# Optimization experiments

Hardware: AMD Instinct MI355X
Metric: run time of the kernel (lower is better)

The kernel has to match this reference:

```python
import jax, jax.numpy as jnp
import numpy as np
import math

N, NF, D, HEADS, LEVELS, POINTS = 1, 2, 256, 8, 4, 4
SPATIAL = np.array([[100, 100], [50, 50], [25, 25], [13, 13]], dtype=np.int32)
LEN_IN = int((SPATIAL[:, 0] * SPATIAL[:, 1]).sum())  # 13294
LEN_Q = LEN_IN


def _grid_init_bias():
    # faithful to MSDeformAttn._reset_parameters
    thetas = np.arange(HEADS, dtype=np.float32) * (2.0 * math.pi / HEADS)
    grid = np.stack([np.cos(thetas), np.sin(thetas)], -1)
    grid = grid / np.abs(grid).max(-1, keepdims=True)
    grid = np.tile(grid.reshape(HEADS, 1, 1, 2), (1, LEVELS, POINTS, 1))
    for i in range(POINTS):
        grid[:, :, i, :] *= i + 1
    return grid.reshape(-1).astype(np.float32)  # [HEADS*LEVELS*POINTS*2]


def setup_inputs() -> dict:
    key = jax.random.key(0)
    ks = jax.random.split(key, 8)
    lsi = np.concatenate([[0], np.cumsum(SPATIAL[:, 0] * SPATIAL[:, 1])[:-1]]).astype(np.int32)
    s = 1.0 / math.sqrt(D)
    return {
        "query": jax.random.normal(ks[0], (N, NF, LEN_Q, D), jnp.float32),
        "reference_points": jax.random.uniform(ks[1], (N, LEN_Q, LEVELS, 2), jnp.float32),
        "input_flatten": jax.random.normal(ks[2], (N, NF, LEN_IN, D), jnp.float32),
        "input_spatial_shapes": jnp.asarray(SPATIAL),
        "input_level_start_index": jnp.asarray(lsi),
        "Wv": jax.random.normal(ks[3], (D, D), jnp.float32) * s,
        "bv": jnp.zeros((D,), jnp.float32),
        "Woff": jax.random.normal(ks[4], (D, HEADS * LEVELS * POINTS * 2), jnp.float32) * 0.01,
        "boff": jnp.asarray(_grid_init_bias()),
        "Wattn": jax.random.normal(ks[5], (D, HEADS * LEVELS * POINTS), jnp.float32) * 0.02,
        "battn": jnp.zeros((HEADS * LEVELS * POINTS,), jnp.float32),
        "Wout": jax.random.normal(ks[6], (D, D), jnp.float32) * s,
        "bout": jnp.zeros((D,), jnp.float32),
    }


def ms_deform_attn_core(value, spatial_shapes, level_start_index, loc, attn):
    """value: [B, Lin, H, Dh]; loc: [B, Lq, H, L, P, 2] in [0,1]; attn: [B, Lq, H, L, P].
    Bilinear sampling matches F.grid_sample(align_corners=False, padding_mode='zeros')
    applied to grid = 2*loc - 1, i.e. pixel coord = loc*size - 0.5."""
    B, Lin, Hn, Dh = value.shape
    Lq, L, P = loc.shape[1], loc.shape[3], loc.shape[4]
    val_t = value.transpose(0, 2, 1, 3)  # [B, H, Lin, Dh]
    out = jnp.zeros((B, Lq, Hn, Dh), value.dtype)
    for l in range(L):
        Hl = spatial_shapes[l, 0]
        Wl = spatial_shapes[l, 1]
        start = level_start_index[l]
        x = loc[:, :, :, l, :, 0] * Wl - 0.5  # [B, Lq, H, P]
        y = loc[:, :, :, l, :, 1] * Hl - 0.5
        x0 = jnp.floor(x)
        y0 = jnp.floor(y)
        lx, ly = x - x0, y - y0
        x0i = x0.astype(jnp.int32)
        y0i = y0.astype(jnp.int32)
        sampled = jnp.zeros((B, Lq, Hn, P, Dh), value.dtype)
        corners = [(0, 0, (1 - lx) * (1 - ly)), (0, 1, lx * (1 - ly)),
                   (1, 0, (1 - lx) * ly), (1, 1, lx * ly)]
        for dy, dx, w in corners:
            xi = x0i + dx
            yi = y0i + dy
            valid = (xi >= 0) & (xi < Wl) & (yi >= 0) & (yi < Hl)
            idx = start + jnp.clip(yi, 0, Hl - 1) * Wl + jnp.clip(xi, 0, Wl - 1)
            idx_t = idx.transpose(0, 2, 1, 3).reshape(B, Hn, Lq * P)  # [B, H, Lq*P]
            v = jnp.take_along_axis(val_t, idx_t[:, :, :, None], axis=2)  # [B, H, Lq*P, Dh]
            v = v.reshape(B, Hn, Lq, P, Dh).transpose(0, 2, 1, 3, 4)  # [B, Lq, H, P, Dh]
            sampled = sampled + jnp.where(valid, w, 0.0)[..., None] * v
        out = out + jnp.einsum('blhp,blhpd->blhd', attn[:, :, :, l, :], sampled)
    return out.reshape(B, Lq, Hn * Dh)


def reference(query, reference_points, input_flatten, input_spatial_shapes,
              input_level_start_index, Wv, bv, Woff, boff, Wattn, battn, Wout, bout):
    n, nf, Lq, d = query.shape
    Lin = input_flatten.shape[2]
    Dh = d // HEADS
    value = (input_flatten @ Wv + bv).reshape(n * nf, Lin, HEADS, Dh)
    off = (query @ Woff + boff).reshape(n, nf, Lq, HEADS, LEVELS, POINTS, 2)
    aw = (query @ Wattn + battn).reshape(n, nf, Lq, HEADS, LEVELS * POINTS)
    aw = jax.nn.softmax(aw, axis=-1).reshape(n, nf, Lq, HEADS, LEVELS, POINTS)
    # offset normalizer: [W, H] per level
    norm = jnp.stack([input_spatial_shapes[:, 1], input_spatial_shapes[:, 0]], -1).astype(query.dtype)
    # reference_points: [n, Lq, L, 2] -> broadcast with offsets [n, nf, Lq, H, L, P, 2]
    loc = reference_points[:, None, :, None, :, None, :] + off / norm[None, None, None, None, :, None, :]
    loc = loc.reshape(n * nf, Lq, HEADS, LEVELS, POINTS, 2)
    aw = aw.reshape(n * nf, Lq, HEADS, LEVELS, POINTS)
    out = ms_deform_attn_core(value, input_spatial_shapes, input_level_start_index, loc, aw)
    out = out.reshape(n, nf, Lq, d)
    return out @ Wout + bout
```

## Files before the change

### kernel.cpp

```cpp
#include <hip/hip_runtime.h>
#include <math.h>

#define LEN_Q 13294
#define LEN_IN 13294
#define NFRAMES 2
#define MTOT (LEN_Q * NFRAMES)
#define HEADS 8
#define LEVELS 4
#define POINTS 4

typedef __attribute__((ext_vector_type(8))) short short8;
typedef __attribute__((ext_vector_type(4))) float f32x4;
typedef __attribute__((ext_vector_type(2))) float f32x2;
typedef __attribute__((ext_vector_type(2))) unsigned int uint2v;
typedef __attribute__((ext_vector_type(4))) unsigned int uint4v;

__device__ __forceinline__ unsigned short f2bf(float x) {
    unsigned u = __builtin_bit_cast(unsigned, x);
    unsigned r = (u + 0x7fffu + ((u >> 16) & 1u)) >> 16;
    return (unsigned short)r;
}
__device__ __forceinline__ float bf2f(unsigned short b) {
    return __builtin_bit_cast(float, (unsigned)b << 16);
}
__device__ __forceinline__ float bfl(unsigned u) {
    return __builtin_bit_cast(float, u << 16);
}
__device__ __forceinline__ float bfh(unsigned u) {
    return __builtin_bit_cast(float, u & 0xffff0000u);
}
__device__ __forceinline__ short8 pack8(f32x4 x0, f32x4 x1) {
    short8 p;
    p[0]=(short)f2bf(x0.x); p[1]=(short)f2bf(x0.y); p[2]=(short)f2bf(x0.z); p[3]=(short)f2bf(x0.w);
    p[4]=(short)f2bf(x1.x); p[5]=(short)f2bf(x1.y); p[6]=(short)f2bf(x1.z); p[7]=(short)f2bf(x1.w);
    return p;
}

__device__ __forceinline__ void gld_lds16(const unsigned short* g, unsigned short* l) {
    __builtin_amdgcn_global_load_lds(
        (const __attribute__((address_space(1))) void*)g,
        (__attribute__((address_space(3))) void*)l, 16, 0, 0);
}

__device__ __forceinline__ void stage_tile(const unsigned short* __restrict__ g,
                                           unsigned short* lds, int t) {
    const unsigned short* ga = g + (t >> 2) * 256 + (t & 3) * 8;
    gld_lds16(ga, lds + t * 8);
    gld_lds16(ga + 64 * 256, lds + 2048 + t * 8);
}

#define CONV_BLOCKS 2048
__global__ __launch_bounds__(256) void prep_all(
    const float* __restrict__ Wv,  const float* __restrict__ Woff,
    const float* __restrict__ Wat, const float* __restrict__ Wout,
    unsigned short* __restrict__ wvT,
    unsigned short* __restrict__ woaT,
    unsigned short* __restrict__ woutT,
    const float* __restrict__ a, const float* __restrict__ b,
    unsigned short* __restrict__ oa, unsigned short* __restrict__ ob)
{
    const int blk = blockIdx.x;
    const int k = threadIdx.x;
    if (blk < 896) {
        const float* src; unsigned short* dst; int N; int n;
        if (blk < 256)      { src = Wv;   dst = wvT;          N = 256; n = blk; }
        else if (blk < 512) { src = Woff; dst = woaT;         N = 256; n = blk - 256; }
        else if (blk < 640) { src = Wat;  dst = woaT + 65536; N = 128; n = blk - 512; }
        else                { src = Wout; dst = woutT;        N = 256; n = blk - 640; }
        dst[(size_t)n * 256 + k] = f2bf(src[(size_t)k * N + n]);
        return;
    }
    size_t gid = (size_t)(blk - 896) * 256 + k;
    size_t stride = (size_t)CONV_BLOCKS * 256;
    const size_t n8 = (size_t)MTOT * 256 / 8;
    for (size_t i = gid; i < n8; i += stride) {
        size_t off = i * 8;
        f32x4 x0 = *(const f32x4*)(a + off);
        f32x4 x1 = *(const f32x4*)(a + off + 4);
        *(short8*)(oa + off) = pack8(x0, x1);
        f32x4 y0 = *(const f32x4*)(b + off);
        f32x4 y1 = *(const f32x4*)(b + off + 4);
        *(short8*)(ob + off) = pack8(y0, y1);
    }
}

#define CSTR 136
__global__ __launch_bounds__(256) void gemm_fused5(
    const unsigned short* __restrict__ A16v,
    const unsigned short* __restrict__ A16q,
    const unsigned short* __restrict__ BTv,
    const unsigned short* __restrict__ BToa,
    const float* __restrict__ bv,
    const float* __restrict__ boff,
    const float* __restrict__ battn,
    unsigned short* __restrict__ vdup,
    unsigned short* __restrict__ off16,
    unsigned short* __restrict__ at16,
    int M)
{
    __shared__ __align__(16) unsigned char shraw[24576];
    unsigned short* As = (unsigned short*)shraw;
    unsigned short* Bs = (unsigned short*)(shraw + 8192);
    unsigned short* Cs = (unsigned short*)shraw;

    const int t = threadIdx.x;
    const int w = t >> 6;
    const int L = t & 63;

    const int bid = blockIdx.x;
    const int xcd = bid & 7;
    const int kk = bid >> 3;
    const int nt = kk % 5;
    const int m0 = ((kk / 5) * 8 + xcd) * 64;

    const unsigned short* Abase = ((nt < 2) ? A16v : A16q) + (size_t)m0 * 256;
    const unsigned short* Bbase = (nt < 2) ? (BTv + (size_t)nt * 128 * 256)
                                           : (BToa + (size_t)(nt - 2) * 128 * 256);

    const int mq = (w & 1) * 32;
    const int nq = (w >> 1) * 64;
    const int lr = L & 15;
    const int kq = (L >> 4) * 8;

    f32x4 acc[2][4];
    #pragma unroll
    for (int i = 0; i < 2; ++i)
        #pragma unroll
        for (int j = 0; j < 4; ++j) acc[i][j] = (f32x4){0.f, 0.f, 0.f, 0.f};

    gld_lds16(Abase + (t >> 2) * 256 + (t & 3) * 8, As + t * 8);
    stage_tile(Bbase, Bs, t);

    #pragma unroll
    for (int ks = 0; ks < 8; ++ks) {
        const int cur = ks & 1;
        __syncthreads();
        if (ks < 7) {
            gld_lds16(Abase + (ks + 1) * 32 + (t >> 2) * 256 + (t & 3) * 8,
                      As + (cur ^ 1) * 2048 + t * 8);
            stage_tile(Bbase + (ks + 1) * 32, Bs + (cur ^ 1) * 4096, t);
        }
        short8 af[2], bf[4];
        #pragma unroll
        for (int i = 0; i < 2; ++i)
            af[i] = *(const short8*)&As[cur * 2048 + (mq + i * 16 + lr) * 32 + kq];
        #pragma unroll
        for (int j = 0; j < 4; ++j)
            bf[j] = *(const short8*)&Bs[cur * 4096 + (nq + j * 16 + lr) * 32 + kq];
        #pragma unroll
        for (int i = 0; i < 2; ++i)
            #pragma unroll
            for (int j = 0; j < 4; ++j)
                acc[i][j] = __builtin_amdgcn_mfma_f32_16x16x32_bf16(af[i], bf[j], acc[i][j], 0, 0, 0);
    }

    __syncthreads();

    const int rr = (L >> 4) * 4;
    {
        float bj[4];
        #pragma unroll
        for (int j = 0; j < 4; ++j) {
            int colg = nt * 128 + nq + j * 16 + lr;
            bj[j] = (colg < 256) ? bv[colg]
                  : (colg < 512) ? boff[colg - 256] : battn[colg - 512];
        }
        #pragma unroll
        for (int i = 0; i < 2; ++i)
            #pragma unroll
            for (int r = 0; r < 4; ++r) {
                int mloc = mq + i * 16 + rr + r;
                #pragma unroll
                for (int j = 0; j < 4; ++j)
                    Cs[mloc * CSTR + nq + j * 16 + lr] = f2bf(acc[i][j][r] + bj[j]);
            }
    }
    __syncthreads();

    if (nt < 2) {
        #pragma unroll
        for (int it = 0; it < 4; ++it) {
            int idx = it * 256 + t;
            int row = idx >> 4;
            int rem = idx & 15;
            int hh_loc = rem >> 2;
            int cc = rem & 3;
            int m = m0 + row;
            if (m < M) {
                int fr = (m >= LEN_Q) ? 1 : 0;
                int e = m - fr * LEN_Q;
                int hh = nt * 4 + hh_loc;
                uint4v v = *(const uint4v*)&Cs[row * CSTR + hh_loc * 32 + cc * 8];
                size_t eb = ((size_t)(fr * 8 + hh) * (LEN_IN + 1) + e) * 64;
                *(uint4v*)&vdup[eb + cc * 8] = v;
                if (e > 0) *(uint4v*)&vdup[eb - 64 + 32 + cc * 8] = v;
            }
        }
    } else if (nt < 4) {
        #pragma unroll
        for (int it = 0; it < 4; ++it) {
            int idx = it * 256 + t;
            int row = idx >> 4;
            int c16 = idx & 15;
            int m = m0 + row;
            if (m < M) {
                uint4v v = *(const uint4v*)&Cs[row * CSTR + c16 * 8];
                *(uint4v*)&off16[(size_t)m * 256 + (nt - 2) * 128 + c16 * 8] = v;
            }
        }
    } else {
        #pragma unroll
        for (int it = 0; it < 4; ++it) {
            int idx = it * 256 + t;
            int row = idx >> 4;
            int c16 = idx & 15;
            int m = m0 + row;
            if (m < M) {
                uint4v v = *(const uint4v*)&Cs[row * CSTR + c16 * 8];
                *(uint4v*)&at16[(size_t)m * 128 + c16 * 8] = v;
            }
        }
    }
}

#define OSTR 132
__global__ __launch_bounds__(256) void gemm_out4(
    const unsigned short* __restrict__ A,
    const unsigned short* __restrict__ BT,
    const float* __restrict__ bias,
    float* __restrict__ C,
    int M)
{
    __shared__ __align__(16) unsigned char raw[64 * OSTR * 4];
    unsigned short* As = (unsigned short*)raw;
    unsigned short* Bs = (unsigned short*)(raw + 8192);
    float* Cs = (float*)raw;

    const int t = threadIdx.x;
    const int w = t >> 6;
    const int L = t & 63;

    const int bid = blockIdx.x;
    const int xcd = bid & 7;
    const int kk = bid >> 3;
    const int nt = kk & 1;
    const int m0 = (((kk >> 1) * 8) + xcd) * 64;
    const int n0 = nt * 128;

    const unsigned short* Abase = A + (size_t)m0 * 256;
    const unsigned short* Bbase = BT + (size_t)n0 * 256;

    const int mq = (w & 1) * 32;
    const int nq = (w >> 1) * 64;
    const int lr = L & 15;
    const int kq = (L >> 4) * 8;

    f32x4 acc[2][4];
    #pragma unroll
    for (int i = 0; i < 2; ++i)
        #pragma unroll
        for (int j = 0; j < 4; ++j) acc[i][j] = (f32x4){0.f, 0.f, 0.f, 0.f};

    gld_lds16(Abase + (t >> 2) * 256 + (t & 3) * 8, As + t * 8);
    stage_tile(Bbase, Bs, t);

    #pragma unroll
    for (int ks = 0; ks < 8; ++ks) {
        const int cur = ks & 1;
        __syncthreads();
        if (ks < 7) {
            gld_lds16(Abase + (ks + 1) * 32 + (t >> 2) * 256 + (t & 3) * 8,
                      As + (cur ^ 1) * 2048 + t * 8);
            stage_tile(Bbase + (ks + 1) * 32, Bs + (cur ^ 1) * 4096, t);
        }
        short8 af[2], bf[4];
        #pragma unroll
        for (int i = 0; i < 2; ++i)
            af[i] = *(const short8*)&As[cur * 2048 + (mq + i * 16 + lr) * 32 + kq];
        #pragma unroll
        for (int j = 0; j < 4; ++j)
            bf[j] = *(const short8*)&Bs[cur * 4096 + (nq + j * 16 + lr) * 32 + kq];
        #pragma unroll
        for (int i = 0; i < 2; ++i)
            #pragma unroll
            for (int j = 0; j < 4; ++j)
                acc[i][j] = __builtin_amdgcn_mfma_f32_16x16x32_bf16(af[i], bf[j], acc[i][j], 0, 0, 0);
    }

    __syncthreads();

    const int rr = (L >> 4) * 4;
    {
        float bj[4];
        #pragma unroll
        for (int j = 0; j < 4; ++j) bj[j] = bias[n0 + nq + j * 16 + lr];
        #pragma unroll
        for (int i = 0; i < 2; ++i)
            #pragma unroll
            for (int r = 0; r < 4; ++r) {
                int mloc = mq + i * 16 + rr + r;
                #pragma unroll
                for (int j = 0; j < 4; ++j)
                    Cs[mloc * OSTR + nq + j * 16 + lr] = acc[i][j][r] + bj[j];
            }
    }
    __syncthreads();

    #pragma unroll
    for (int it = 0; it < 8; ++it) {
        int idx = it * 256 + t;
        int row = idx >> 5;
        int c = idx & 31;
        int m = m0 + row;
        if (m < M) {
            f32x4 v = *(const f32x4*)&Cs[row * OSTR + c * 4];
            *(f32x4*)(C + (size_t)m * 256 + n0 + c * 4) = v;
        }
    }
}

__global__ __launch_bounds__(256) void sample12(
    const unsigned short* __restrict__ vdup,
    const unsigned short* __restrict__ off,
    const unsigned short* __restrict__ attn,
    const float* __restrict__ refpts,
    const int*   __restrict__ spatial,
    const int*   __restrict__ lsi,
    unsigned short* __restrict__ samp)
{
    const int b = blockIdx.x;
    const int h = b & 7;
    const int chunk = b >> 3;
    const int t = threadIdx.x;
    const int rl = t >> 3;
    const int j = t & 7;

    int row = chunk * 32 + rl;
    const bool valid = row < MTOT;
    if (row > MTOT - 1) row = MTOT - 1;
    const int frame = row >= LEN_Q ? 1 : 0;
    const int q = row - frame * LEN_Q;

    __shared__ float w_s[32][68];
    __shared__ int   b_s[32][20];

    uint2v ov = *(const uint2v*)(off + (size_t)row * 256 + h * 32 + j * 4);
    unsigned av = *(const unsigned*)(attn + (size_t)row * 128 + h * 16 + j * 2);
    float t0 = bf2f((unsigned short)(av & 0xffffu));
    float t1 = bf2f((unsigned short)(av >> 16));

    float m = fmaxf(t0, t1);
    #pragma unroll
    for (int d = 1; d < 8; d <<= 1) m = fmaxf(m, __shfl_xor(m, d));
    float e0 = __expf(t0 - m);
    float e1 = __expf(t1 - m);
    float s = e0 + e1;
    #pragma unroll
    for (int d = 1; d < 8; d <<= 1) s += __shfl_xor(s, d);
    float inv = 1.f / s;
    float wt01[2] = { e0 * inv, e1 * inv };

    {
        const int l = j >> 1;
        const int Hl = spatial[l * 2], Wl = spatial[l * 2 + 1];
        const int start = lsi[l];
        const int slab = (frame * 8 + h) * (LEN_IN + 1);
        const float rx = refpts[((size_t)q * LEVELS + l) * 2];
        const float ry = refpts[((size_t)q * LEVELS + l) * 2 + 1];
        #pragma unroll
        for (int i = 0; i < 2; ++i) {
            const int lp = 2 * j + i;
            unsigned sel = (i == 0) ? ov.x : ov.y;
            float ox = bf2f((unsigned short)(sel & 0xffffu));
            float oy = bf2f((unsigned short)(sel >> 16));
            float locx = rx + ox * __builtin_amdgcn_rcpf((float)Wl);
            float locy = ry + oy * __builtin_amdgcn_rcpf((float)Hl);
            float wt = wt01[i];
            float x = locx * (float)Wl - 0.5f;
            float y = locy * (float)Hl - 0.5f;
            float x0f = floorf(x), y0f = floorf(y);
            float lx = x - x0f, ly = y - y0f;
            int x0 = (int)x0f, y0 = (int)y0f;
            int xbase = min(max(x0, 0), Wl - 2);
            int ybase = min(max(y0, 0), Hl - 2);
            float wxe0 = (x0 == xbase) ? (1.f - lx) : ((x0 == -1) ? lx : 0.f);
            float wxe1 = (x0 == xbase) ? lx : ((x0 == Wl - 1) ? (1.f - lx) : 0.f);
            float wye0 = (y0 == ybase) ? (1.f - ly) : ((y0 == -1) ? ly : 0.f);
            float wye1 = (y0 == ybase) ? ly : ((y0 == Hl - 1) ? (1.f - ly) : 0.f);
            b_s[rl][lp] = (slab + start + ybase * Wl + xbase) * 128;
            f32x4 wv;
            wv.x = wt * wxe0 * wye0;
            wv.y = wt * wxe0 * wye1;
            wv.z = wt * wxe1 * wye0;
            wv.w = wt * wxe1 * wye1;
            *(f32x4*)&w_s[rl][lp * 4] = wv;
        }
    }
    __syncthreads();

    const char* vb = (const char*)vdup;
    const unsigned lane16 = (unsigned)(j * 16);
    const int hi2 = ((j >> 2) & 1) * 2;
    int ystr[4];
    #pragma unroll
    for (int l2 = 0; l2 < 4; ++l2) ystr[l2] = spatial[l2 * 2 + 1] * 128;

    f32x2  wbuf[3][2];
    uint4v vbuf[3][4];
    auto fetch = [&](int buf, int g) {
        wbuf[buf][0] = *(const f32x2*)&w_s[rl][(2 * g) * 4 + hi2];
        wbuf[buf][1] = *(const f32x2*)&w_s[rl][(2 * g + 1) * 4 + hi2];
        int b0 = b_s[rl][2 * g];
        int b1 = b_s[rl][2 * g + 1];
        int ys = ystr[g >> 1];
        vbuf[buf][0] = *(const uint4v*)(vb + (unsigned)b0 + lane16);
        vbuf[buf][1] = *(const uint4v*)(vb + (unsigned)(b0 + ys) + lane16);
        vbuf[buf][2] = *(const uint4v*)(vb + (unsigned)b1 + lane16);
        vbuf[buf][3] = *(const uint4v*)(vb + (unsigned)(b1 + ys) + lane16);
    };

    f32x2 a2[4];
    #pragma unroll
    for (int k = 0; k < 4; ++k) a2[k] = (f32x2){0.f, 0.f};

    fetch(0, 0);
    fetch(1, 1);
    #pragma unroll
    for (int g = 0; g < 8; ++g) {
        const int cur = g % 3;
        if (g < 6) fetch((g + 2) % 3, g + 2);
        #pragma unroll
        for (int p = 0; p < 2; ++p) {
            f32x2 wp = wbuf[cur][p];
            f32x2 wy0 = (f32x2){wp.x, wp.x};
            f32x2 wy1 = (f32x2){wp.y, wp.y};
            uint4v v0 = vbuf[cur][p * 2];
            uint4v v1 = vbuf[cur][p * 2 + 1];
            #pragma unroll
            for (int k = 0; k < 4; ++k) {
                f32x2 x0 = (f32x2){bfl(v0[k]), bfh(v0[k])};
                f32x2 x1 = (f32x2){bfl(v1[k]), bfh(v1[k])};
                a2[k] = __builtin_elementwise_fma(wy0, x0, a2[k]);
                a2[k] = __builtin_elementwise_fma(wy1, x1, a2[k]);
            }
        }
    }

    float a[8];
    #pragma unroll
    for (int k = 0; k < 4; ++k) { a[2 * k] = a2[k].x; a[2 * k + 1] = a2[k].y; }

    #pragma unroll
    for (int k = 0; k < 8; ++k) a[k] += __shfl_xor(a[k], 4);

    if (valid && hi2 == 0) {
        uint4v o;
        #pragma unroll
        for (int k = 0; k < 4; ++k)
            o[k] = (unsigned)f2bf(a[2 * k]) | ((unsigned)f2bf(a[2 * k + 1]) << 16);
        *(uint4v*)(samp + (size_t)row * 256 + h * 32 + (j & 3) * 8) = o;
    }
}

extern "C" void kernel_launch(void* const* d_in, const int* in_sizes, int n_in,
                              void* d_out, int out_size, void* d_ws, size_t ws_size,
                              hipStream_t stream)
{
    const float* query   = (const float*)d_in[0];
    const float* refpts  = (const float*)d_in[1];
    const float* inflat  = (const float*)d_in[2];
    const int*   spatial = (const int*)d_in[3];
    const int*   lsi     = (const int*)d_in[4];
    const float* Wv      = (const float*)d_in[5];
    const float* bv      = (const float*)d_in[6];
    const float* Woff    = (const float*)d_in[7];
    const float* boff    = (const float*)d_in[8];
    const float* Wattn   = (const float*)d_in[9];
    const float* battn   = (const float*)d_in[10];
    const float* Wout    = (const float*)d_in[11];
    const float* bout    = (const float*)d_in[12];

    unsigned short* ws = (unsigned short*)d_ws;
    const size_t MR = (size_t)MTOT * 256;
    const size_t VDUP = (size_t)16 * (LEN_IN + 1) * 64;
    unsigned short* vdup   = ws;
    unsigned short* off16  = vdup + VDUP;
    unsigned short* at16   = off16 + MR;
    unsigned short* samp16 = at16 + (size_t)MTOT * 128;
    unsigned short* a16v   = samp16 + MR;
    unsigned short* a16q   = a16v + MR;
    unsigned short* wvT    = a16q + MR;
    unsigned short* woaT   = wvT + 65536;
    unsigned short* woutT  = woaT + 98304;

    dim3 blk256(256);

    hipLaunchKernelGGL(prep_all, dim3(896 + CONV_BLOCKS), blk256, 0, stream,
                       Wv, Woff, Wattn, Wout, wvT, woaT, woutT,
                       inflat, query, a16v, a16q);

    hipLaunchKernelGGL(gemm_fused5, dim3(2080), blk256, 0, stream,
                       a16v, a16q, wvT, woaT, bv, boff, battn,
                       vdup, off16, at16, MTOT);

    hipLaunchKernelGGL(sample12, dim3(6648), blk256, 0, stream,
                       vdup, off16, at16, refpts, spatial, lsi, samp16);

    hipLaunchKernelGGL(gemm_out4, dim3(832), blk256, 0, stream,
                       samp16, woutT, bout, (float*)d_out, MTOT);
}
```

Baseline: 187.0 us.

## Fuse fp32-to-bf16 input conversion into projection GEMM and shrink sampler prefetch depth

```diff
diff --git a/kernel.cpp b/kernel.cpp
--- a/kernel.cpp
+++ b/kernel.cpp
@@ -49,45 +49,28 @@
     gld_lds16(ga + 64 * 256, lds + 2048 + t * 8);
 }
 
-#define CONV_BLOCKS 2048
-__global__ __launch_bounds__(256) void prep_all(
+__global__ __launch_bounds__(256) void prep_weights(
     const float* __restrict__ Wv,  const float* __restrict__ Woff,
     const float* __restrict__ Wat, const float* __restrict__ Wout,
     unsigned short* __restrict__ wvT,
     unsigned short* __restrict__ woaT,
-    unsigned short* __restrict__ woutT,
-    const float* __restrict__ a, const float* __restrict__ b,
-    unsigned short* __restrict__ oa, unsigned short* __restrict__ ob)
+    unsigned short* __restrict__ woutT)
 {
-    const int blk = blockIdx.x;
+    const int b = blockIdx.x;
     const int k = threadIdx.x;
-    if (blk < 896) {
-        const float* src; unsigned short* dst; int N; int n;
-        if (blk < 256)      { src = Wv;   dst = wvT;          N = 256; n = blk; }
-        else if (blk < 512) { src = Woff; dst = woaT;         N = 256; n = blk - 256; }
-        else if (blk < 640) { src = Wat;  dst = woaT + 65536; N = 128; n = blk - 512; }
-        else                { src = Wout; dst = woutT;        N = 256; n = blk - 640; }
-        dst[(size_t)n * 256 + k] = f2bf(src[(size_t)k * N + n]);
-        return;
-    }
-    size_t gid = (size_t)(blk - 896) * 256 + k;
-    size_t stride = (size_t)CONV_BLOCKS * 256;
-    const size_t n8 = (size_t)MTOT * 256 / 8;
-    for (size_t i = gid; i < n8; i += stride) {
-        size_t off = i * 8;
-        f32x4 x0 = *(const f32x4*)(a + off);
-        f32x4 x1 = *(const f32x4*)(a + off + 4);
-        *(short8*)(oa + off) = pack8(x0, x1);
-        f32x4 y0 = *(const f32x4*)(b + off);
-        f32x4 y1 = *(const f32x4*)(b + off + 4);
-        *(short8*)(ob + off) = pack8(y0, y1);
-    }
+    const float* src; unsigned short* dst; int N; int n;
+    if (b < 256)      { src = Wv;   dst = wvT;          N = 256; n = b; }
+    else if (b < 512) { src = Woff; dst = woaT;         N = 256; n = b - 256; }
+    else if (b < 640) { src = Wat;  dst = woaT + 65536; N = 128; n = b - 512; }
+    else              { src = Wout; dst = woutT;        N = 256; n = b - 640; }
+    dst[(size_t)n * 256 + k] = f2bf(src[(size_t)k * N + n]);
 }
 
 #define CSTR 136
-__global__ __launch_bounds__(256) void gemm_fused5(
-    const unsigned short* __restrict__ A16v,
-    const unsigned short* __restrict__ A16q,
+#define ASTRIDE 264
+__global__ __launch_bounds__(256) void gemm_fused6(
+    const float* __restrict__ Aval,
+    const float* __restrict__ Aq,
     const unsigned short* __restrict__ BTv,
     const unsigned short* __restrict__ BToa,
     const float* __restrict__ bv,
@@ -98,9 +81,9 @@
     unsigned short* __restrict__ at16,
     int M)
 {
-    __shared__ __align__(16) unsigned char shraw[24576];
-    unsigned short* As = (unsigned short*)shraw;
-    unsigned short* Bs = (unsigned short*)(shraw + 8192);
+    __shared__ __align__(16) unsigned char shraw[50176];
+    unsigned short* Afull = (unsigned short*)shraw;
+    unsigned short* Bs = (unsigned short*)(shraw + 33792);
     unsigned short* Cs = (unsigned short*)shraw;
 
     const int t = threadIdx.x;
@@ -113,7 +96,7 @@
     const int nt = kk % 5;
     const int m0 = ((kk / 5) * 8 + xcd) * 64;
 
-    const unsigned short* Abase = ((nt < 2) ? A16v : A16q) + (size_t)m0 * 256;
+    const float* Af = (nt < 2) ? Aval : Aq;
     const unsigned short* Bbase = (nt < 2) ? (BTv + (size_t)nt * 128 * 256)
                                            : (BToa + (size_t)(nt - 2) * 128 * 256);
 
@@ -128,22 +111,35 @@
         #pragma unroll
         for (int j = 0; j < 4; ++j) acc[i][j] = (f32x4){0.f, 0.f, 0.f, 0.f};
 
-    gld_lds16(Abase + (t >> 2) * 256 + (t & 3) * 8, As + t * 8);
     stage_tile(Bbase, Bs, t);
+
+    {
+        const int r = t >> 2;
+        const int c0 = (t & 3) * 64;
+        int arow = m0 + r; if (arow > M - 1) arow = M - 1;
+        const float* pa = Af + (size_t)arow * 256 + c0;
+        unsigned short* da = &Afull[r * ASTRIDE + c0];
+        #pragma unroll
+        for (int cc = 0; cc < 64; cc += 16) {
+            f32x4 v0 = *(const f32x4*)(pa + cc);
+            f32x4 v1 = *(const f32x4*)(pa + cc + 4);
+            f32x4 v2 = *(const f32x4*)(pa + cc + 8);
+            f32x4 v3 = *(const f32x4*)(pa + cc + 12);
+            *(short8*)(da + cc)     = pack8(v0, v1);
+            *(short8*)(da + cc + 8) = pack8(v2, v3);
+        }
+    }
 
     #pragma unroll
     for (int ks = 0; ks < 8; ++ks) {
         const int cur = ks & 1;
         __syncthreads();
-        if (ks < 7) {
-            gld_lds16(Abase + (ks + 1) * 32 + (t >> 2) * 256 + (t & 3) * 8,
-                      As + (cur ^ 1) * 2048 + t * 8);
+        if (ks < 7)
             stage_tile(Bbase + (ks + 1) * 32, Bs + (cur ^ 1) * 4096, t);
-        }
         short8 af[2], bf[4];
         #pragma unroll
         for (int i = 0; i < 2; ++i)
-            af[i] = *(const short8*)&As[cur * 2048 + (mq + i * 16 + lr) * 32 + kq];
+            af[i] = *(const short8*)&Afull[(mq + i * 16 + lr) * ASTRIDE + ks * 32 + kq];
         #pragma unroll
         for (int j = 0; j < 4; ++j)
             bf[j] = *(const short8*)&Bs[cur * 4096 + (nq + j * 16 + lr) * 32 + kq];
@@ -319,7 +315,7 @@
     }
 }
 
-__global__ __launch_bounds__(256) void sample12(
+__global__ __launch_bounds__(256) void sample11(
     const unsigned short* __restrict__ vdup,
     const unsigned short* __restrict__ off,
     const unsigned short* __restrict__ attn,
@@ -405,8 +401,8 @@
     #pragma unroll
     for (int l2 = 0; l2 < 4; ++l2) ystr[l2] = spatial[l2 * 2 + 1] * 128;
 
-    f32x2  wbuf[3][2];
-    uint4v vbuf[3][4];
+    f32x2  wbuf[2][2];
+    uint4v vbuf[2][4];
     auto fetch = [&](int buf, int g) {
         wbuf[buf][0] = *(const f32x2*)&w_s[rl][(2 * g) * 4 + hi2];
         wbuf[buf][1] = *(const f32x2*)&w_s[rl][(2 * g + 1) * 4 + hi2];
@@ -424,11 +420,10 @@
     for (int k = 0; k < 4; ++k) a2[k] = (f32x2){0.f, 0.f};
 
     fetch(0, 0);
-    fetch(1, 1);
     #pragma unroll
     for (int g = 0; g < 8; ++g) {
-        const int cur = g % 3;
-        if (g < 6) fetch((g + 2) % 3, g + 2);
+        const int cur = g & 1;
+        if (g < 7) fetch(cur ^ 1, g + 1);
         #pragma unroll
         for (int p = 0; p < 2; ++p) {
             f32x2 wp = wbuf[cur][p];
@@ -487,23 +482,20 @@
     unsigned short* off16  = vdup + VDUP;
     unsigned short* at16   = off16 + MR;
     unsigned short* samp16 = at16 + (size_t)MTOT * 128;
-    unsigned short* a16v   = samp16 + MR;
-    unsigned short* a16q   = a16v + MR;
-    unsigned short* wvT    = a16q + MR;
+    unsigned short* wvT    = samp16 + MR;
     unsigned short* woaT   = wvT + 65536;
     unsigned short* woutT  = woaT + 98304;
 
     dim3 blk256(256);
 
-    hipLaunchKernelGGL(prep_all, dim3(896 + CONV_BLOCKS), blk256, 0, stream,
-                       Wv, Woff, Wattn, Wout, wvT, woaT, woutT,
-                       inflat, query, a16v, a16q);
-
-    hipLaunchKernelGGL(gemm_fused5, dim3(2080), blk256, 0, stream,
-                       a16v, a16q, wvT, woaT, bv, boff, battn,
+    hipLaunchKernelGGL(prep_weights, dim3(896), blk256, 0, stream,
+                       Wv, Woff, Wattn, Wout, wvT, woaT, woutT);
+
+    hipLaunchKernelGGL(gemm_fused6, dim3(2080), blk256, 0, stream,
+                       inflat, query, wvT, woaT, bv, boff, battn,
                        vdup, off16, at16, MTOT);
 
-    hipLaunchKernelGGL(sample12, dim3(6648), blk256, 0, stream,
+    hipLaunchKernelGGL(sample11, dim3(6648), blk256, 0, stream,
                        vdup, off16, at16, refpts, spatial, lsi, samp16);
 
     hipLaunchKernelGGL(gemm_out4, dim3(832), blk256, 0, stream,
```

Result: no change. 190.3 us (+1.8%).
